# Kernel tuning notes

Measured on AMD Instinct MI355X. Metric: run time of the kernel, lower is better.

Reference implementation:

```python
import jax, jax.numpy as jnp
import numpy as np

B, T, D, H, O = 256, 512, 128, 128, 64


def setup_inputs() -> dict:
    key = jax.random.key(0)
    ks = jax.random.split(key, 10)
    s = 1.0 / np.sqrt(H)
    u = lambda k, shape: jax.random.uniform(k, shape, jnp.float32, -s, s)
    return {
        "x": jax.random.normal(ks[0], (B, T, D), jnp.float32),
        "W_ih": u(ks[1], (4 * H, D)),   # torch gate order: i, f, g, o
        "W_hh": u(ks[2], (4 * H, H)),
        "b_ih": u(ks[3], (4 * H,)),
        "b_hh": u(ks[4], (4 * H,)),
        "W1": u(ks[5], (H, H)),
        "b1": u(ks[6], (H,)),
        "W2": u(ks[7], (O, H)),
        "b2": u(ks[8], (O,)),
    }


def lstm_scan(x, W_ih, W_hh, b_ih, b_hh):
    b, t, _ = x.shape
    h4 = W_hh.shape[0] // 4
    # precompute input contribution for all timesteps (one big GEMM)
    xg = jnp.einsum('btd,gd->btg', x, W_ih) + b_ih + b_hh  # (B,T,4H)
    xg = jnp.swapaxes(xg, 0, 1)  # (T,B,4H) for scan over time

    def step(carry, xg_t):
        h, c = carry
        g = xg_t + h @ W_hh.T  # (B,4H)
        i, f, gg, o = jnp.split(g, 4, axis=-1)
        i = jax.nn.sigmoid(i)
        f = jax.nn.sigmoid(f)
        gg = jnp.tanh(gg)
        o = jax.nn.sigmoid(o)
        c = f * c + i * gg
        h = o * jnp.tanh(c)
        return (h, c), h

    h0 = jnp.zeros((b, h4), x.dtype)
    c0 = jnp.zeros((b, h4), x.dtype)
    _, hs = jax.lax.scan(step, (h0, c0), xg)  # hs: (T,B,H)
    return jnp.swapaxes(hs, 0, 1)  # (B,T,H), matching torch batch_first


def reference(x, W_ih, W_hh, b_ih, b_hh, W1, b1, W2, b2):
    b, t, _ = x.shape
    h = lstm_scan(x, W_ih, W_hh, b_ih, b_hh)          # (B,T,H)
    hflat = h.reshape(-1, h.shape[-1])                 # (B*T,H), b-major (as torch)
    hflat = hflat @ W1.T + b1
    y = hflat @ W2.T + b2                              # (B*T,O)
    # faithful to original: reshape flattened b-major rows as (T,B,O), take [-1]
    y = y.reshape(t, b, -1)
    return y[-1]                                       # (B,O)
```

## Files before the change

### kernel.cpp

```cpp
#include <hip/hip_runtime.h>
#include <math.h>

#define BB 256
#define TT 512
#define DD 128
#define HH 128
#define GG 512
#define OO 64

#define LOG2E    1.44269504088896340736f
#define TWOLOG2E 2.88539008177792681472f

typedef _Float16 half8 __attribute__((ext_vector_type(8)));
typedef float    f32x4 __attribute__((ext_vector_type(4)));

__global__ __launch_bounds__(512) void xgpack_kernel(
    const float* __restrict__ x,
    const float* __restrict__ W_ih,
    const float* __restrict__ b_ih,
    const float* __restrict__ b_hh,
    const float* __restrict__ W_hh,
    float* __restrict__ xg,
    _Float16* __restrict__ Wp)
{
    if (blockIdx.x >= TT) {
        const int g = (blockIdx.x - TT) * 512 + threadIdx.x;
        const int fid = g >> 6, l = g & 63;
        const int w = fid >> 5, rem = fid & 31, nt = rem >> 2, kt = rem & 3;
        const int quad = l >> 4, col = l & 15;
        const int row = (nt >> 1) * 128 + (nt & 1) * 16 + w * 32 + col;
        const int off = kt * 32 + quad * 8;
        const float ws = ((row >> 7) == 2) ? TWOLOG2E : LOG2E;
        const float* s = W_hh + row * HH + off;
        _Float16* d = Wp + (size_t)g * 8;
#pragma unroll
        for (int i = 0; i < 8; i++) d[i] = (_Float16)(s[i] * ws);
        return;
    }

    const int t = blockIdx.x;
    const int g = threadIdx.x;

    __shared__ __align__(16) float xs[DD];
    if (g < DD) xs[g] = x[(255 * TT + t) * DD + g];
    __syncthreads();

    const float4* __restrict__ wrow = (const float4*)(W_ih + g * DD);
    const float4* __restrict__ xv   = (const float4*)xs;

    float a0 = 0.f, a1 = 0.f, a2 = 0.f, a3 = 0.f;
#pragma unroll
    for (int i = 0; i < DD / 4; i += 4) {
        float4 w0 = wrow[i + 0], w1 = wrow[i + 1], w2 = wrow[i + 2], w3 = wrow[i + 3];
        float4 h0 = xv[i + 0],  h1 = xv[i + 1],  h2 = xv[i + 2],  h3 = xv[i + 3];
        a0 += w0.x * h0.x + w0.y * h0.y + w0.z * h0.z + w0.w * h0.w;
        a1 += w1.x * h1.x + w1.y * h1.y + w1.z * h1.z + w1.w * h1.w;
        a2 += w2.x * h2.x + w2.y * h2.y + w2.z * h2.z + w2.w * h2.w;
        a3 += w3.x * h3.x + w3.y * h3.y + w3.z * h3.z + w3.w * h3.w;
    }
    const float scale = ((g >> 7) == 2) ? TWOLOG2E : LOG2E;
    const float val = ((a0 + a1) + (a2 + a3) + b_ih[g] + b_hh[g]) * scale;
    xg[t * GG + (g & 127) * 4 + (g >> 7)] = val;
}

__global__
__attribute__((amdgpu_flat_work_group_size(256, 256), amdgpu_waves_per_eu(1, 1)))
void scan_kernel(
    const _Float16* __restrict__ Wp,
    const float* __restrict__ xgp,
    float* __restrict__ hs)
{
    const int tid  = threadIdx.x;
    const int lane = tid & 63;
    const int w    = tid >> 6;
    const int col  = lane & 15;
    const int quad = lane >> 4;
    const int wbase = w * 32;
    const bool sel  = (lane >= 32);
    const int jsel  = wbase + (sel ? 16 : 0) + col;
    const int aoff  = quad * 8;
    const bool wr   = (quad == 0) || (quad == 3);

    __shared__ __align__(16) _Float16 h_lds[2][HH];
    __shared__ __align__(16) float hs_l[BB * HH];

#define BLOADP(nt, kt) \
    half8 B##nt##_##kt = *(const half8*)(Wp + (((w * 32 + (nt) * 4 + (kt)) * 64 + lane) * 8));
#define FOR_KT(X, nt) X(nt, 0) X(nt, 1) X(nt, 2) X(nt, 3)
#define FOR_NT(X) FOR_KT(X, 0) FOR_KT(X, 1) FOR_KT(X, 2) FOR_KT(X, 3) \
                  FOR_KT(X, 4) FOR_KT(X, 5) FOR_KT(X, 6) FOR_KT(X, 7)
    FOR_NT(BLOADP)

    asm volatile("" : "+v"(B0_0), "+v"(B0_1), "+v"(B0_2), "+v"(B0_3),
                      "+v"(B1_0), "+v"(B1_1), "+v"(B1_2), "+v"(B1_3),
                      "+v"(B2_0), "+v"(B2_1), "+v"(B2_2), "+v"(B2_3),
                      "+v"(B3_0), "+v"(B3_1), "+v"(B3_2), "+v"(B3_3));
    asm volatile("" : "+v"(B4_0), "+v"(B4_1), "+v"(B4_2), "+v"(B4_3),
                      "+v"(B5_0), "+v"(B5_1), "+v"(B5_2), "+v"(B5_3),
                      "+v"(B6_0), "+v"(B6_1), "+v"(B6_2), "+v"(B6_3),
                      "+v"(B7_0), "+v"(B7_1), "+v"(B7_2), "+v"(B7_3));

    if (tid < HH) h_lds[0][tid] = (_Float16)0.f;

    f32x4 Z = {0.f, 0.f, 0.f, 0.f};
    asm volatile("" : "+v"(Z));

    const float* __restrict__ xgl = xgp + jsel * 4;
    f32x4 xg0 = *(const f32x4*)(xgl + 0 * GG);
    f32x4 xg1 = *(const f32x4*)(xgl + 1 * GG);

    float c = 0.f;
    __syncthreads();

#define MM(a, b, cc) __builtin_amdgcn_mfma_f32_16x16x32_f16((a), (b), (cc), 0, 0, 0)
#define STEP(par, XCUR) do {                                                            \
    const int t = t2 + (par);                                                           \
    const _Float16* hl = h_lds[(par)];                                                  \
    half8 A0 = *(const half8*)(hl +  0 + aoff);                                         \
    half8 A1 = *(const half8*)(hl + 32 + aoff);                                         \
    half8 A2 = *(const half8*)(hl + 64 + aoff);                                         \
    half8 A3 = *(const half8*)(hl + 96 + aoff);                                         \
    f32x4 C0, C1, C2, C3, C4, C5, C6, C7;                                               \
    C4 = MM(A0, B4_0, Z);  C5 = MM(A0, B5_0, Z);  C0 = MM(A0, B0_0, Z);                 \
    C1 = MM(A0, B1_0, Z);  C2 = MM(A0, B2_0, Z);  C3 = MM(A0, B3_0, Z);                 \
    C6 = MM(A0, B6_0, Z);  C7 = MM(A0, B7_0, Z);                                        \
    C4 = MM(A1, B4_1, C4); C5 = MM(A1, B5_1, C5); C0 = MM(A1, B0_1, C0);                \
    C1 = MM(A1, B1_1, C1); C2 = MM(A1, B2_1, C2); C3 = MM(A1, B3_1, C3);                \
    C6 = MM(A1, B6_1, C6); C7 = MM(A1, B7_1, C7);                                       \
    C4 = MM(A2, B4_2, C4); C5 = MM(A2, B5_2, C5); C0 = MM(A2, B0_2, C0);                \
    C1 = MM(A2, B1_2, C1); C2 = MM(A2, B2_2, C2); C3 = MM(A2, B3_2, C3);                \
    C6 = MM(A2, B6_2, C6); C7 = MM(A2, B7_2, C7);                                       \
    C4 = MM(A3, B4_3, C4); C5 = MM(A3, B5_3, C5); C0 = MM(A3, B0_3, C0);                \
    C1 = MM(A3, B1_3, C1); C2 = MM(A3, B2_3, C2); C3 = MM(A3, B3_3, C3);                \
    C6 = MM(A3, B6_3, C6); C7 = MM(A3, B7_3, C7);                                       \
                   \
    float pi = (sel ? C1[0] : C0[0]) + (XCUR).x;                                        \
    float pf = (sel ? C3[0] : C2[0]) + (XCUR).y;                                        \
    float pg = (sel ? C5[0] : C4[0]) + (XCUR).z;                                        \
    float po = (sel ? C7[0] : C6[0]) + (XCUR).w;                                        \
              \
              \
    (XCUR) = *(const f32x4*)(xgl + ((t + 2) & (TT - 1)) * GG);                          \
    float iv = __builtin_amdgcn_rcpf(1.0f + __builtin_amdgcn_exp2f(-pi));               \
    float fv = __builtin_amdgcn_rcpf(1.0f + __builtin_amdgcn_exp2f(-pf));               \
    float ov = __builtin_amdgcn_rcpf(1.0f + __builtin_amdgcn_exp2f(-po));               \
    float Eg = __builtin_amdgcn_exp2f(fabsf(pg));                                       \
    float rg = __builtin_amdgcn_rcpf(Eg + 1.0f);                                        \
    float T  = copysignf(TWOLOG2E, pg);                                                 \
    float gvs = fmaf(-2.0f * T, rg, T);                     \
    c = fmaf(fv, c, iv * gvs);                      \
    float Ec = __builtin_amdgcn_exp2f(fabsf(c));                                        \
    float rc = __builtin_amdgcn_rcpf(Ec + 1.0f);                                        \
    float Ao = copysignf(ov, c);                                                        \
    float hval = fmaf(-2.0f * Ao, rc, Ao);                                              \
    if (wr) {                                                                           \
        h_lds[1 - (par)][jsel] = (_Float16)hval;                                        \
        hs_l[(t & (BB - 1)) * HH + jsel] = hval;          \
    }                                                                                   \
    asm volatile("s_waitcnt lgkmcnt(0)\n\ts_barrier" ::: "memory");                     \
} while (0)

    for (int t2 = 0; t2 < TT; t2 += 2) {
        STEP(0, xg0);
        STEP(1, xg1);
    }
#undef STEP
#undef MM

    const f32x4* s = (const f32x4*)hs_l;
    f32x4* d = (f32x4*)hs;
#pragma unroll 4
    for (int i = tid; i < BB * HH / 4; i += 256) d[i] = s[i];
}

__global__ __launch_bounds__(128) void mlp_kernel(
    const float* __restrict__ hs,
    const float* __restrict__ W1,
    const float* __restrict__ b1,
    const float* __restrict__ W2,
    const float* __restrict__ b2,
    float* __restrict__ out)
{
    const int r = blockIdx.x;
    const int j = threadIdx.x;

    __shared__ __align__(16) float hsh[HH];
    __shared__ __align__(16) float z[HH];

    hsh[j] = hs[r * HH + j];
    __syncthreads();

    {
        const float4* __restrict__ wrow = (const float4*)(W1 + j * HH);
        const float4* __restrict__ hv   = (const float4*)hsh;
        float acc = b1[j];
#pragma unroll
        for (int i = 0; i < 32; i++) {
            float4 ww = wrow[i], h = hv[i];
            acc += ww.x * h.x + ww.y * h.y + ww.z * h.z + ww.w * h.w;
        }
        z[j] = acc;
    }
    __syncthreads();

    if (j < OO) {
        const float4* __restrict__ wrow = (const float4*)(W2 + j * HH);
        const float4* __restrict__ zv   = (const float4*)z;
        float acc = b2[j];
#pragma unroll
        for (int i = 0; i < 32; i++) {
            float4 ww = wrow[i], zz = zv[i];
            acc += ww.x * zz.x + ww.y * zz.y + ww.z * zz.z + ww.w * zz.w;
        }
        out[r * OO + j] = acc;
    }
}

extern "C" void kernel_launch(void* const* d_in, const int* in_sizes, int n_in,
                              void* d_out, int out_size, void* d_ws, size_t ws_size,
                              hipStream_t stream) {
    const float* x    = (const float*)d_in[0];
    const float* W_ih = (const float*)d_in[1];
    const float* W_hh = (const float*)d_in[2];
    const float* b_ih = (const float*)d_in[3];
    const float* b_hh = (const float*)d_in[4];
    const float* W1   = (const float*)d_in[5];
    const float* b1   = (const float*)d_in[6];
    const float* W2   = (const float*)d_in[7];
    const float* b2   = (const float*)d_in[8];
    float* out = (float*)d_out;

    float*    xg = (float*)d_ws;
    float*    hs = xg + TT * GG;
    _Float16* Wp = (_Float16*)(hs + BB * HH);

    xgpack_kernel<<<TT + 16, 512, 0, stream>>>(x, W_ih, b_ih, b_hh, W_hh, xg, Wp);
    scan_kernel<<<1, 256, 0, stream>>>(Wp, xg, hs);
    mlp_kernel<<<BB, 128, 0, stream>>>(hs, W1, b1, W2, b2, out);
}
```

Measured before the change: 331.1 us.

## Rotate K-chunk order so each wave prefetches its own h slice before barrier

Each wave now walks the recurrent GEMM's K chunks starting with the 32 h values it produced itself. It can load that fragment right after its own LDS write completes, before the workgroup barrier. The W_hh register fragments are permuted to match the rotated order. The fp32 hs_l history store is deferred by one step so it is off the critical path between the h computation and the barrier, with a final store and sync added after the loop. This shortens the per-timestep serial chain, at the cost of an extra live register fragment and slightly more index arithmetic.

```diff
diff --git a/kernel.cpp b/kernel.cpp
--- a/kernel.cpp
+++ b/kernel.cpp
@@ -81,11 +81,16 @@
     const int aoff  = quad * 8;
     const bool wr   = (quad == 0) || (quad == 3);
 
+    const int offA0 = ((w + 0) & 3) * 32 + aoff;
+    const int offA1 = ((w + 1) & 3) * 32 + aoff;
+    const int offA2 = ((w + 2) & 3) * 32 + aoff;
+    const int offA3 = ((w + 3) & 3) * 32 + aoff;
+
     __shared__ __align__(16) _Float16 h_lds[2][HH];
     __shared__ __align__(16) float hs_l[BB * HH];
 
-#define BLOADP(nt, kt) \
-    half8 B##nt##_##kt = *(const half8*)(Wp + (((w * 32 + (nt) * 4 + (kt)) * 64 + lane) * 8));
+#define BLOADP(nt, s) \
+    half8 B##nt##_##s = *(const half8*)(Wp + (((w * 32 + (nt) * 4 + ((w + (s)) & 3)) * 64 + lane) * 8));
 #define FOR_KT(X, nt) X(nt, 0) X(nt, 1) X(nt, 2) X(nt, 3)
 #define FOR_NT(X) FOR_KT(X, 0) FOR_KT(X, 1) FOR_KT(X, 2) FOR_KT(X, 3) \
                   FOR_KT(X, 4) FOR_KT(X, 5) FOR_KT(X, 6) FOR_KT(X, 7)
@@ -110,16 +115,21 @@
     f32x4 xg1 = *(const f32x4*)(xgl + 1 * GG);
 
     float c = 0.f;
-    __syncthreads();
+    float hval_prev = 0.f;
+    __syncthreads();
+
+    half8 A0c = *(const half8*)(&h_lds[0][0] + offA0);
 
 #define MM(a, b, cc) __builtin_amdgcn_mfma_f32_16x16x32_f16((a), (b), (cc), 0, 0, 0)
 #define STEP(par, XCUR) do {                                                            \
     const int t = t2 + (par);                                                           \
     const _Float16* hl = h_lds[(par)];                                                  \
-    half8 A0 = *(const half8*)(hl +  0 + aoff);                                         \
-    half8 A1 = *(const half8*)(hl + 32 + aoff);                                         \
-    half8 A2 = *(const half8*)(hl + 64 + aoff);                                         \
-    half8 A3 = *(const half8*)(hl + 96 + aoff);                                         \
+    half8 A0 = A0c;                                                                     \
+    half8 A1 = *(const half8*)(hl + offA1);                                             \
+    half8 A2 = *(const half8*)(hl + offA2);                                             \
+    half8 A3 = *(const half8*)(hl + offA3);                                             \
+                    \
+    if (wr) hs_l[((t - 1) & (BB - 1)) * HH + jsel] = hval_prev;                         \
     f32x4 C0, C1, C2, C3, C4, C5, C6, C7;                                               \
     C4 = MM(A0, B4_0, Z);  C5 = MM(A0, B5_0, Z);  C0 = MM(A0, B0_0, Z);                 \
     C1 = MM(A0, B1_0, Z);  C2 = MM(A0, B2_0, Z);  C3 = MM(A0, B3_0, Z);                 \
@@ -138,8 +148,7 @@
     float pf = (sel ? C3[0] : C2[0]) + (XCUR).y;                                        \
     float pg = (sel ? C5[0] : C4[0]) + (XCUR).z;                                        \
     float po = (sel ? C7[0] : C6[0]) + (XCUR).w;                                        \
-              \
-              \
+                 \
     (XCUR) = *(const f32x4*)(xgl + ((t + 2) & (TT - 1)) * GG);                          \
     float iv = __builtin_amdgcn_rcpf(1.0f + __builtin_amdgcn_exp2f(-pi));               \
     float fv = __builtin_amdgcn_rcpf(1.0f + __builtin_amdgcn_exp2f(-pf));               \
@@ -153,11 +162,12 @@
     float rc = __builtin_amdgcn_rcpf(Ec + 1.0f);                                        \
     float Ao = copysignf(ov, c);                                                        \
     float hval = fmaf(-2.0f * Ao, rc, Ao);                                              \
-    if (wr) {                                                                           \
-        h_lds[1 - (par)][jsel] = (_Float16)hval;                                        \
-        hs_l[(t & (BB - 1)) * HH + jsel] = hval;          \
-    }                                                                                   \
-    asm volatile("s_waitcnt lgkmcnt(0)\n\ts_barrier" ::: "memory");                     \
+    if (wr) h_lds[1 - (par)][jsel] = (_Float16)hval;                                    \
+    hval_prev = hval;                                                                   \
+    asm volatile("s_waitcnt lgkmcnt(0)" ::: "memory");                                  \
+                  \
+    A0c = *(const half8*)(&h_lds[1 - (par)][0] + offA0);                                \
+    asm volatile("s_barrier" ::: "memory");                                             \
 } while (0)
 
     for (int t2 = 0; t2 < TT; t2 += 2) {
@@ -166,6 +176,9 @@
     }
 #undef STEP
 #undef MM
+
+    if (wr) hs_l[(BB - 1) * HH + jsel] = hval_prev;
+    __syncthreads();
 
     const f32x4* s = (const f32x4*)hs_l;
     f32x4* d = (f32x4*)hs;
```

Result: no change. 326.0 us (-1.5%).
